# Performance work log

Hardware: AMD Instinct MI355X
Metric: run time of the kernel (lower is better)

Reference implementation:

```python
import jax, jax.numpy as jnp
import numpy as np
import math

N_USER = 50000
N_ITEM = 50000
E_PER = 400000
F_IN = 128
F_OUT = 128
H = 4
D = F_OUT // H  # 32
NUM_ET = 2  # edge types: 0 = user->item, 1 = item->user


def setup_inputs() -> dict:
    key = jax.random.key(0)
    ks = jax.random.split(key, 16)
    s = 0.05  # weight scale to keep activations tame
    return {
        "x_user": jax.random.normal(ks[0], (N_USER, F_IN), jnp.float32),
        "x_item": jax.random.normal(ks[1], (N_ITEM, F_IN), jnp.float32),
        "W_kqv_user": jax.random.normal(ks[2], (F_IN, 3 * F_OUT), jnp.float32) * s,
        "b_kqv_user": jax.random.normal(ks[3], (3 * F_OUT,), jnp.float32) * s,
        "W_kqv_item": jax.random.normal(ks[4], (F_IN, 3 * F_OUT), jnp.float32) * s,
        "b_kqv_item": jax.random.normal(ks[5], (3 * F_OUT,), jnp.float32) * s,
        "Wk_rel": jax.random.normal(ks[6], (H * NUM_ET, D, D), jnp.float32) * s,
        "Wv_rel": jax.random.normal(ks[7], (H * NUM_ET, D, D), jnp.float32) * s,
        "W_out_user": jax.random.normal(ks[8], (F_OUT, F_OUT), jnp.float32) * s,
        "b_out_user": jax.random.normal(ks[9], (F_OUT,), jnp.float32) * s,
        "W_out_item": jax.random.normal(ks[10], (F_OUT, F_OUT), jnp.float32) * s,
        "b_out_item": jax.random.normal(ks[11], (F_OUT,), jnp.float32) * s,
        "skip_user": jnp.ones((1,), jnp.float32),
        "skip_item": jnp.ones((1,), jnp.float32),
        "p_rel_ui": jnp.ones((H,), jnp.float32),
        "p_rel_iu": jnp.ones((H,), jnp.float32),
        "edge_ui": jax.random.randint(ks[12], (2, E_PER), 0, N_USER, dtype=jnp.int32),
        "edge_iu": jax.random.randint(ks[13], (2, E_PER), 0, N_ITEM, dtype=jnp.int32),
    }


def _kqv(x, W, b):
    o = x @ W + b  # [N, 3F]
    k, q, v = o[:, :F_OUT], o[:, F_OUT:2 * F_OUT], o[:, 2 * F_OUT:]
    return (k.reshape(-1, H, D), q.reshape(-1, H, D), v.reshape(-1, H, D))


def _rel(x, Wrel, et):
    # HeteroLinear with type index h*NUM_ET + et per head (is_sorted layout)
    W = Wrel[jnp.arange(H) * NUM_ET + et]  # [H, D, D]
    return jnp.einsum('nhd,hde->nhe', x, W)


def reference(x_user, x_item, W_kqv_user, b_kqv_user, W_kqv_item, b_kqv_item,
              Wk_rel, Wv_rel, W_out_user, b_out_user, W_out_item, b_out_item,
              skip_user, skip_item, p_rel_ui, p_rel_iu, edge_ui, edge_iu):
    ku, qu, vu = _kqv(x_user, W_kqv_user, b_kqv_user)
    ki, qi, vi = _kqv(x_item, W_kqv_item, b_kqv_item)

    # per-edge-type relation transform of K/V (grouped GEMM by head x edge-type)
    k0, v0 = _rel(ku, Wk_rel, 0), _rel(vu, Wv_rel, 0)  # src of user->item
    k1, v1 = _rel(ki, Wk_rel, 1), _rel(vi, Wv_rel, 1)  # src of item->user

    q_all = jnp.concatenate([qu, qi], 0)  # dst offsets: user=0, item=N_USER
    n_tot = N_USER + N_ITEM

    src0, dst0 = edge_ui[0], edge_ui[1] + N_USER
    src1, dst1 = edge_iu[0], edge_iu[1]

    kj = jnp.concatenate([k0[src0], k1[src1]], 0)  # [E, H, D]
    vj = jnp.concatenate([v0[src0], v1[src1]], 0)  # [E, H, D]
    dst = jnp.concatenate([dst0, dst1], 0)         # [E]
    p = jnp.concatenate([jnp.broadcast_to(p_rel_ui, (E_PER, H)),
                         jnp.broadcast_to(p_rel_iu, (E_PER, H))], 0)

    qe = q_all[dst]                                  # [E, H, D]
    alpha = (qe * kj).sum(-1) * p / math.sqrt(D)     # [E, H]

    # segment softmax over destination nodes (PyG softmax: max-shift, +1e-16)
    amax = jax.ops.segment_max(alpha, dst, num_segments=n_tot)
    a = jnp.exp(alpha - amax[dst])
    denom = jax.ops.segment_sum(a, dst, num_segments=n_tot)
    a = a / (denom[dst] + 1e-16)

    out = jax.ops.segment_sum(vj * a[:, :, None], dst, num_segments=n_tot)
    out = out.reshape(n_tot, F_OUT)
    out_u, out_i = out[:N_USER], out[N_USER:]

    g = lambda t: jax.nn.gelu(t, approximate=False)
    a_u = g(out_u) @ W_out_user + b_out_user
    a_i = g(out_i) @ W_out_item + b_out_item

    su = jax.nn.sigmoid(skip_user)  # out_channels == in_channels -> skip blend
    si = jax.nn.sigmoid(skip_item)
    return (su * a_u + (1.0 - su) * x_user,
            si * a_i + (1.0 - si) * x_item)
```

## Files before the change

### kernel.cpp

```cpp
#include <hip/hip_runtime.h>
#include <hip/hip_bf16.h>
#include <math.h>

#define N_USERS 50000
#define N_ITEMS 50000
#define NN      100000
#define E_PER_  400000
#define E_TOT   800000
#define FDIM    128
#define NH      4
#define HD      32
#define SCAN_CHUNK 1024
#define SCAN_NB    ((NN + SCAN_CHUNK - 1) / SCAN_CHUNK)
#define KQV_NB  ((N_USERS + 127) / 128)

typedef __attribute__((ext_vector_type(8))) short bfrag;
typedef __attribute__((ext_vector_type(4))) float f32x4;

__device__ __forceinline__ float gelu_exact(float x) {
    return 0.5f * x * (1.0f + erff(x * 0.70710678118654752f));
}
__device__ __forceinline__ unsigned short f2bf(float f) {
    unsigned u = __float_as_uint(f);
    unsigned r = u + 0x7fffu + ((u >> 16) & 1u);
    return (unsigned short)(r >> 16);
}
__device__ __forceinline__ void unpack8(uint4 u, float* f) {
    f[0] = __uint_as_float(u.x << 16); f[1] = __uint_as_float(u.x & 0xffff0000u);
    f[2] = __uint_as_float(u.y << 16); f[3] = __uint_as_float(u.y & 0xffff0000u);
    f[4] = __uint_as_float(u.z << 16); f[5] = __uint_as_float(u.z & 0xffff0000u);
    f[6] = __uint_as_float(u.w << 16); f[7] = __uint_as_float(u.w & 0xffff0000u);
}

__global__ void prep_kqv(
    const float* __restrict__ W_u, const float* __restrict__ b_u,
    const float* __restrict__ W_i, const float* __restrict__ b_i,
    const float* __restrict__ Wk_rel, const float* __restrict__ Wv_rel,
    unsigned short* __restrict__ Wt_u, float* __restrict__ bias_u,
    unsigned short* __restrict__ Wt_i, float* __restrict__ bias_i)
{
    const int et = blockIdx.x >> 9 ? 1 : (blockIdx.x >= 384);
    const int n = blockIdx.x - et * 384;
    const int k = threadIdx.x;
    const float* W = et ? W_i : W_u;
    const float* b = et ? b_i : b_u;
    unsigned short* Wt = et ? Wt_i : Wt_u;
    float* bias_f = et ? bias_i : bias_u;
    float s;
    if (n < 128) {
        int h = n >> 5, e = n & 31;
        const float* wr = Wk_rel + (size_t)(h * 2 + et) * 1024 + e;
        const float* wc = W + (size_t)k * 384 + h * 32;
        s = 0.f;
        for (int d = 0; d < 32; ++d) s = fmaf(wc[d], wr[d * 32], s);
        if (k == 0) {
            float bs = 0.f;
            for (int d = 0; d < 32; ++d) bs = fmaf(b[h * 32 + d], wr[d * 32], bs);
            bias_f[n] = bs;
        }
    } else if (n < 256) {
        s = W[(size_t)k * 384 + n];
        if (k == 0) bias_f[n] = b[n];
    } else {
        int h = (n - 256) >> 5, e = (n - 256) & 31;
        const float* wr = Wv_rel + (size_t)(h * 2 + et) * 1024 + e;
        const float* wc = W + (size_t)k * 384 + 256 + h * 32;
        s = 0.f;
        for (int d = 0; d < 32; ++d) s = fmaf(wc[d], wr[d * 32], s);
        if (k == 0) {
            float bs = 0.f;
            for (int d = 0; d < 32; ++d) bs = fmaf(b[256 + h * 32 + d], wr[d * 32], bs);
            bias_f[n] = bs;
        }
    }
    Wt[(size_t)n * 128 + k] = f2bf(s);
}

__global__ void prep_wo(
    const float* __restrict__ W_u, unsigned short* __restrict__ Wt_u,
    const float* __restrict__ W_i, unsigned short* __restrict__ Wt_i)
{
    int i = blockIdx.x * blockDim.x + threadIdx.x;
    int side = i >= 128 * 128;
    int j = i - side * 128 * 128;
    if (j >= 128 * 128) return;
    int nrow = j >> 7, k = j & 127;
    const float* W = side ? W_i : W_u;
    unsigned short* Wt = side ? Wt_i : Wt_u;
    Wt[j] = f2bf(W[(size_t)k * 128 + nrow]);
}

__global__ __launch_bounds__(256, 2) void kqv_mfma(
    const float* __restrict__ X_u, const unsigned short* __restrict__ Wt_u,
    const float* __restrict__ bias_u,
    const float* __restrict__ X_i, const unsigned short* __restrict__ Wt_i,
    const float* __restrict__ bias_i,
    unsigned short* __restrict__ kk_b,
    unsigned short* __restrict__ q_b,
    unsigned short* __restrict__ vv_b)
{
    __shared__ unsigned short Xs[128 * 128];
    __shared__ unsigned short Ws[128 * 128];
    const int t = threadIdx.x;
    const int side = blockIdx.x >= KQV_NB;
    const int m0 = (blockIdx.x - side * KQV_NB) * 128;
    const float* X = side ? X_i : X_u;
    const unsigned short* Wt = side ? Wt_i : Wt_u;
    const float* bias = side ? bias_i : bias_u;
    const int side_off = side ? N_USERS : 0;
    const int M = N_USERS;

    for (int c = t; c < 128 * 16; c += 256) {
        int r = c >> 4, sub = c & 15;
        int row = m0 + r;
        float4 a = make_float4(0.f, 0.f, 0.f, 0.f);
        float4 b4 = make_float4(0.f, 0.f, 0.f, 0.f);
        if (row < M) {
            a  = *reinterpret_cast<const float4*>(X + (size_t)row * 128 + sub * 8);
            b4 = *reinterpret_cast<const float4*>(X + (size_t)row * 128 + sub * 8 + 4);
        }
        uint4 pk;
        pk.x = (unsigned)f2bf(a.x)  | ((unsigned)f2bf(a.y)  << 16);
        pk.y = (unsigned)f2bf(a.z)  | ((unsigned)f2bf(a.w)  << 16);
        pk.z = (unsigned)f2bf(b4.x) | ((unsigned)f2bf(b4.y) << 16);
        pk.w = (unsigned)f2bf(b4.z) | ((unsigned)f2bf(b4.w) << 16);
        int dst = r * 256 + ((sub * 16) ^ ((r & 7) << 4));
        *reinterpret_cast<uint4*>(reinterpret_cast<char*>(Xs) + dst) = pk;
    }
    for (int c = t; c < 128 * 16; c += 256) {
        int r = c >> 4, sub = c & 15;
        uint4 v = *reinterpret_cast<const uint4*>(
            reinterpret_cast<const char*>(Wt) + (size_t)r * 256 + sub * 16);
        int dst = r * 256 + ((sub * 16) ^ ((r & 7) << 4));
        *reinterpret_cast<uint4*>(reinterpret_cast<char*>(Ws) + dst) = v;
    }
    __syncthreads();

    const int wave = t >> 6, lane = t & 63;
    const int lr = lane & 15, lg = lane >> 4;

    bfrag am[2][4];
    #pragma unroll
    for (int mt = 0; mt < 2; ++mt)
        #pragma unroll
        for (int ks = 0; ks < 4; ++ks) {
            int row = wave * 32 + mt * 16 + lr;
            int off = row * 256 + ((ks * 64 + lg * 16) ^ ((row & 7) << 4));
            am[mt][ks] = *reinterpret_cast<const bfrag*>(
                reinterpret_cast<const char*>(Xs) + off);
        }

    #pragma unroll
    for (int ch = 0; ch < 3; ++ch) {
        if (ch) {
            __syncthreads();
            for (int c = t; c < 128 * 16; c += 256) {
                int r = c >> 4, sub = c & 15;
                uint4 v = *reinterpret_cast<const uint4*>(
                    reinterpret_cast<const char*>(Wt) + (size_t)(ch * 128 + r) * 256 + sub * 16);
                int dst = r * 256 + ((sub * 16) ^ ((r & 7) << 4));
                *reinterpret_cast<uint4*>(reinterpret_cast<char*>(Ws) + dst) = v;
            }
            __syncthreads();
        }

        f32x4 acc[2][8];
        const f32x4 zero = {0.f, 0.f, 0.f, 0.f};
        #pragma unroll
        for (int mt = 0; mt < 2; ++mt)
            #pragma unroll
            for (int nt = 0; nt < 8; ++nt) acc[mt][nt] = zero;

        #pragma unroll
        for (int nt = 0; nt < 8; ++nt) {
            bfrag bt[4];
            int row = nt * 16 + lr;
            #pragma unroll
            for (int ks = 0; ks < 4; ++ks) {
                int off = row * 256 + ((ks * 64 + lg * 16) ^ ((row & 7) << 4));
                bt[ks] = *reinterpret_cast<const bfrag*>(
                    reinterpret_cast<const char*>(Ws) + off);
            }
            #pragma unroll
            for (int mt = 0; mt < 2; ++mt)
                #pragma unroll
                for (int ks = 0; ks < 4; ++ks)
                    acc[mt][nt] = __builtin_amdgcn_mfma_f32_16x16x32_bf16(
                        am[mt][ks], bt[ks], acc[mt][nt], 0, 0, 0);
        }

        unsigned short* arr = (ch == 0) ? kk_b : (ch == 1) ? q_b : vv_b;
        #pragma unroll
        for (int nt = 0; nt < 8; ++nt) {
            int ic = nt * 16 + lr;
            float bv = bias[ch * 128 + ic];
            #pragma unroll
            for (int mt = 0; mt < 2; ++mt)
                #pragma unroll
                for (int r = 0; r < 4; ++r) {
                    int row = m0 + wave * 32 + mt * 16 + lg * 4 + r;
                    if (row < M)
                        arr[(size_t)(side_off + row) * 128 + ic] = f2bf(acc[mt][nt][r] + bv);
                }
        }
    }
}

__device__ __forceinline__ void edge_src_dst(
    int e, const int* __restrict__ edge_ui, const int* __restrict__ edge_iu,
    int& src, int& dst)
{
    if (e < E_PER_) {
        src = edge_ui[e];
        dst = edge_ui[E_PER_ + e] + N_USERS;
    } else {
        int e2 = e - E_PER_;
        src = N_USERS + edge_iu[e2];
        dst = edge_iu[E_PER_ + e2];
    }
}

__global__ __launch_bounds__(256) void hist_kernel(
    const int* __restrict__ edge_ui, const int* __restrict__ edge_iu,
    int* __restrict__ cnt)
{
    int e = blockIdx.x * blockDim.x + threadIdx.x;
    if (e >= E_TOT) return;
    int src, dst;
    edge_src_dst(e, edge_ui, edge_iu, src, dst);
    atomicAdd(cnt + dst, 1);
}

__global__ __launch_bounds__(256) void scan1_kernel(
    const int* __restrict__ cnt, int* __restrict__ base, int* __restrict__ bsum)
{
    __shared__ int ssum[256];
    const int t = threadIdx.x;
    const int i0 = blockIdx.x * SCAN_CHUNK + t * 4;
    int v[4];
    #pragma unroll
    for (int j = 0; j < 4; ++j) v[j] = (i0 + j < NN) ? cnt[i0 + j] : 0;
    int tsum = v[0] + v[1] + v[2] + v[3];
    ssum[t] = tsum;
    __syncthreads();
    int run = tsum;
    for (int off = 1; off < 256; off <<= 1) {
        int o = (t >= off) ? ssum[t - off] : 0;
        __syncthreads();
        run += o;
        ssum[t] = run;
        __syncthreads();
    }
    int excl = run - tsum;
    int p = excl;
    #pragma unroll
    for (int j = 0; j < 4; ++j) {
        if (i0 + j < NN) base[i0 + j] = p;
        p += v[j];
    }
    if (t == 255) bsum[blockIdx.x] = run;
}

__global__ void scan2_kernel(int* __restrict__ bsum)
{
    const int lane = threadIdx.x;
    int a = (lane < SCAN_NB) ? bsum[lane] : 0;
    int b = (64 + lane < SCAN_NB) ? bsum[64 + lane] : 0;
    int sa = a, sb = b;
    for (int off = 1; off < 64; off <<= 1) {
        int ta = __shfl_up(sa, off);
        int tb = __shfl_up(sb, off);
        if (lane >= off) { sa += ta; sb += tb; }
    }
    int total0 = __shfl(sa, 63);
    if (lane < SCAN_NB) bsum[lane] = sa - a;
    if (64 + lane < SCAN_NB) bsum[64 + lane] = total0 + sb - b;
}

__global__ __launch_bounds__(256) void scan3_kernel(
    int* __restrict__ base, const int* __restrict__ bsum, int* __restrict__ cursor)
{
    int i = blockIdx.x * blockDim.x + threadIdx.x;
    if (i >= NN) return;
    int b = base[i] + bsum[i >> 10];
    base[i] = b;
    cursor[i] = b;
}

__global__ __launch_bounds__(256) void fill_kernel(
    const int* __restrict__ edge_ui, const int* __restrict__ edge_iu,
    int* __restrict__ cursor, int* __restrict__ esrc)
{
    int e = blockIdx.x * blockDim.x + threadIdx.x;
    if (e >= E_TOT) return;
    int src, dst;
    edge_src_dst(e, edge_ui, edge_iu, src, dst);
    int pos = atomicAdd(cursor + dst, 1);
    esrc[pos] = src;
}

__global__ __launch_bounds__(256) void attn_fused(
    const unsigned short* __restrict__ q_b, const unsigned short* __restrict__ kk_b,
    const unsigned short* __restrict__ vv_b,
    const int* __restrict__ base, const int* __restrict__ cnt,
    const int* __restrict__ esrc,
    const float* __restrict__ p_ui, const float* __restrict__ p_iu,
    unsigned short* __restrict__ oa)
{
    const int wid  = (blockIdx.x * blockDim.x + threadIdx.x) >> 6;
    const int lane = threadIdx.x & 63;
    const int nw   = (gridDim.x * blockDim.x) >> 6;
    const int g    = lane >> 4;
    const int p    = lane & 15;
    const int h    = p >> 2;
    const float rsd = 0.17677669529663687f;
    const float pu = p_ui[h], pi = p_iu[h];

    for (int n = wid; n < NN; n += nw) {
        const float pr = (n >= N_USERS) ? pu : pi;
        float qf[8];
        unpack8(*reinterpret_cast<const uint4*>(q_b + (size_t)n * 128 + p * 8), qf);
        float m = -INFINITY, l = 0.f;
        float acc[8] = {0.f, 0.f, 0.f, 0.f, 0.f, 0.f, 0.f, 0.f};
        const int s0 = base[n], c = cnt[n];

        if (c > 0) {
            bool valid = g < c;
            int src = esrc[s0 + (valid ? g : 0)];
            uint4 k4 = *reinterpret_cast<const uint4*>(kk_b + (size_t)src * 128 + p * 8);
            uint4 v4 = *reinterpret_cast<const uint4*>(vv_b + (size_t)src * 128 + p * 8);

            for (int j = 0; j < c; j += 4) {
                uint4 k4n, v4n;
                bool validn = false;
                if (j + 4 < c) {
                    int jn = j + 4 + g;
                    validn = jn < c;
                    int srcn = esrc[s0 + (validn ? jn : 0)];
                    k4n = *reinterpret_cast<const uint4*>(kk_b + (size_t)srcn * 128 + p * 8);
                    v4n = *reinterpret_cast<const uint4*>(vv_b + (size_t)srcn * 128 + p * 8);
                }

                float kf[8];
                unpack8(k4, kf);
                float s = qf[0] * kf[0];
                #pragma unroll
                for (int i = 1; i < 8; ++i) s = fmaf(qf[i], kf[i], s);
                s += __shfl_xor(s, 1);
                s += __shfl_xor(s, 2);
                float al = valid ? s * pr * rsd : -INFINITY;
                float amx = fmaxf(al, __shfl_xor(al, 16));
                amx = fmaxf(amx, __shfl_xor(amx, 32));
                if (__any(amx > m + 8.f)) {
                    float nm = fmaxf(m, amx);
                    float scale = __expf(m - nm);
                    l *= scale;
                    #pragma unroll
                    for (int i = 0; i < 8; ++i) acc[i] *= scale;
                    m = nm;
                }
                float w = __expf(al - m);
                l += w;
                float vf[8];
                unpack8(v4, vf);
                #pragma unroll
                for (int i = 0; i < 8; ++i) acc[i] = fmaf(w, vf[i], acc[i]);

                k4 = k4n; v4 = v4n; valid = validn;
            }
        }

        l += __shfl_xor(l, 16); l += __shfl_xor(l, 32);
        #pragma unroll
        for (int i = 0; i < 8; ++i) {
            acc[i] += __shfl_xor(acc[i], 16);
            acc[i] += __shfl_xor(acc[i], 32);
        }
        if (g == 0) {
            float inv = 1.0f / (l + 1e-16f);
            uint4 pk;
            unsigned o[4];
            #pragma unroll
            for (int i = 0; i < 4; ++i) {
                float lo = gelu_exact(acc[2 * i] * inv);
                float hi = gelu_exact(acc[2 * i + 1] * inv);
                o[i] = (unsigned)f2bf(lo) | ((unsigned)f2bf(hi) << 16);
            }
            pk.x = o[0]; pk.y = o[1]; pk.z = o[2]; pk.w = o[3];
            *reinterpret_cast<uint4*>(oa + (size_t)n * 128 + p * 8) = pk;
        }
    }
}

__global__ __launch_bounds__(256, 2) void final_mfma(
    const unsigned short* __restrict__ oa,
    const float* __restrict__ x_u, const unsigned short* __restrict__ Wt_u,
    const float* __restrict__ bo_u, const float* __restrict__ skip_u,
    const float* __restrict__ x_i, const unsigned short* __restrict__ Wt_i,
    const float* __restrict__ bo_i, const float* __restrict__ skip_i,
    float* __restrict__ out)
{
    __shared__ unsigned short Ws[128 * 128];
    __shared__ unsigned short Gs[128 * 128];
    const int t = threadIdx.x;
    const int side = blockIdx.x >= KQV_NB;
    const int m0 = (blockIdx.x - side * KQV_NB) * 128;
    const float* x = side ? x_i : x_u;
    const unsigned short* Wt = side ? Wt_i : Wt_u;
    const float* bo = side ? bo_i : bo_u;
    const float* skip = side ? skip_i : skip_u;
    const int row_off = side ? N_USERS : 0;
    const int M = N_USERS;

    for (int c = t; c < 128 * 16; c += 256) {
        int r = c >> 4, sub = c & 15;
        uint4 v = *reinterpret_cast<const uint4*>(
            reinterpret_cast<const char*>(Wt) + r * 256 + sub * 16);
        int dst = r * 256 + ((sub * 16) ^ ((r & 7) << 4));
        *reinterpret_cast<uint4*>(reinterpret_cast<char*>(Ws) + dst) = v;
    }
    for (int c = t; c < 128 * 16; c += 256) {
        int r = c >> 4, sub = c & 15;
        int row = m0 + r;
        uint4 v = make_uint4(0u, 0u, 0u, 0u);
        if (row < M)
            v = *reinterpret_cast<const uint4*>(
                reinterpret_cast<const char*>(oa) + (size_t)(row_off + row) * 256 + sub * 16);
        int dst = r * 256 + ((sub * 16) ^ ((r & 7) << 4));
        *reinterpret_cast<uint4*>(reinterpret_cast<char*>(Gs) + dst) = v;
    }
    __syncthreads();

    const int wave = t >> 6, lane = t & 63;
    const int lr = lane & 15, lg = lane >> 4;

    bfrag am[2][4];
    #pragma unroll
    for (int mt = 0; mt < 2; ++mt)
        #pragma unroll
        for (int ks = 0; ks < 4; ++ks) {
            int row = wave * 32 + mt * 16 + lr;
            int off = row * 256 + ((ks * 64 + lg * 16) ^ ((row & 7) << 4));
            am[mt][ks] = *reinterpret_cast<const bfrag*>(
                reinterpret_cast<const char*>(Gs) + off);
        }

    f32x4 acc[2][8];
    const f32x4 zero = {0.f, 0.f, 0.f, 0.f};
    #pragma unroll
    for (int mt = 0; mt < 2; ++mt)
        #pragma unroll
        for (int nt = 0; nt < 8; ++nt) acc[mt][nt] = zero;

    #pragma unroll
    for (int nt = 0; nt < 8; ++nt) {
        bfrag bt[4];
        int row = nt * 16 + lr;
        #pragma unroll
        for (int ks = 0; ks < 4; ++ks) {
            int off = row * 256 + ((ks * 64 + lg * 16) ^ ((row & 7) << 4));
            bt[ks] = *reinterpret_cast<const bfrag*>(
                reinterpret_cast<const char*>(Ws) + off);
        }
        #pragma unroll
        for (int mt = 0; mt < 2; ++mt)
            #pragma unroll
            for (int ks = 0; ks < 4; ++ks)
                acc[mt][nt] = __builtin_amdgcn_mfma_f32_16x16x32_bf16(
                    am[mt][ks], bt[ks], acc[mt][nt], 0, 0, 0);
    }

    const float sg = 1.0f / (1.0f + expf(-skip[0]));
    #pragma unroll
    for (int nt = 0; nt < 8; ++nt) {
        int col = nt * 16 + lr;
        float bv = bo[col];
        #pragma unroll
        for (int mt = 0; mt < 2; ++mt)
            #pragma unroll
            for (int r = 0; r < 4; ++r) {
                int row = m0 + wave * 32 + mt * 16 + lg * 4 + r;
                if (row < M) {
                    float xv = x[(size_t)row * 128 + col];
                    out[(size_t)(row_off + row) * 128 + col] =
                        sg * (acc[mt][nt][r] + bv) + (1.f - sg) * xv;
                }
            }
    }
}

extern "C" void kernel_launch(void* const* d_in, const int* in_sizes, int n_in,
                              void* d_out, int out_size, void* d_ws, size_t ws_size,
                              hipStream_t stream)
{
    const float* x_user     = (const float*)d_in[0];
    const float* x_item     = (const float*)d_in[1];
    const float* W_kqv_user = (const float*)d_in[2];
    const float* b_kqv_user = (const float*)d_in[3];
    const float* W_kqv_item = (const float*)d_in[4];
    const float* b_kqv_item = (const float*)d_in[5];
    const float* Wk_rel     = (const float*)d_in[6];
    const float* Wv_rel     = (const float*)d_in[7];
    const float* W_out_user = (const float*)d_in[8];
    const float* b_out_user = (const float*)d_in[9];
    const float* W_out_item = (const float*)d_in[10];
    const float* b_out_item = (const float*)d_in[11];
    const float* skip_user  = (const float*)d_in[12];
    const float* skip_item  = (const float*)d_in[13];
    const float* p_ui       = (const float*)d_in[14];
    const float* p_iu       = (const float*)d_in[15];
    const int*   edge_ui    = (const int*)d_in[16];
    const int*   edge_iu    = (const int*)d_in[17];

    const size_t NODE_F = (size_t)NN * FDIM;
    char* w = (char*)d_ws;
    size_t off = 0;
    auto alloc = [&](size_t bytes) {
        char* p = w + off;
        off += (bytes + 255) & ~(size_t)255;
        return p;
    };
    unsigned short* q_b   = (unsigned short*)alloc(NODE_F * 2);
    unsigned short* kk_b  = (unsigned short*)alloc(NODE_F * 2);
    unsigned short* vv_b  = (unsigned short*)alloc(NODE_F * 2);
    unsigned short* oa_b  = (unsigned short*)alloc(NODE_F * 2);
    int* esrc   = (int*)alloc((size_t)E_TOT * 4);
    int* cnt    = (int*)alloc((size_t)NN * 4);
    int* base   = (int*)alloc((size_t)NN * 4);
    int* cursor = (int*)alloc((size_t)NN * 4);
    int* bsum   = (int*)alloc((size_t)SCAN_NB * 4);
    unsigned short* Wt_u   = (unsigned short*)alloc(384 * 128 * 2);
    unsigned short* Wt_i   = (unsigned short*)alloc(384 * 128 * 2);
    float*          bias_u = (float*)alloc(384 * 4);
    float*          bias_i = (float*)alloc(384 * 4);
    unsigned short* Wo_u   = (unsigned short*)alloc(128 * 128 * 2);
    unsigned short* Wo_i   = (unsigned short*)alloc(128 * 128 * 2);

    prep_kqv<<<768, 128, 0, stream>>>(W_kqv_user, b_kqv_user, W_kqv_item, b_kqv_item,
                                      Wk_rel, Wv_rel, Wt_u, bias_u, Wt_i, bias_i);
    prep_wo<<<128, 256, 0, stream>>>(W_out_user, Wo_u, W_out_item, Wo_i);

    kqv_mfma<<<2 * KQV_NB, 256, 0, stream>>>(x_user, Wt_u, bias_u,
                                             x_item, Wt_i, bias_i,
                                             kk_b, q_b, vv_b);

    hipMemsetAsync(cnt, 0, (size_t)NN * 4, stream);
    hist_kernel<<<(E_TOT + 255) / 256, 256, 0, stream>>>(edge_ui, edge_iu, cnt);
    scan1_kernel<<<SCAN_NB, 256, 0, stream>>>(cnt, base, bsum);
    scan2_kernel<<<1, 64, 0, stream>>>(bsum);
    scan3_kernel<<<(NN + 255) / 256, 256, 0, stream>>>(base, bsum, cursor);
    fill_kernel<<<(E_TOT + 255) / 256, 256, 0, stream>>>(edge_ui, edge_iu, cursor, esrc);

    attn_fused<<<2048, 256, 0, stream>>>(q_b, kk_b, vv_b, base, cnt, esrc,
                                         p_ui, p_iu, oa_b);

    final_mfma<<<2 * KQV_NB, 256, 0, stream>>>(
        oa_b, x_user, Wo_u, b_out_user, skip_user,
        x_item, Wo_i, b_out_item, skip_item, (float*)d_out);
}
```

Measured before the change: 282.0 us.

## Pre-swizzle weights into MFMA fragment order and drop LDS staging in GEMMs

Weights are pre-packed into per-lane MFMA fragment order, so the kqv and final GEMM kernels load A and B fragments straight from global memory into registers instead of staging through shared memory with barriers. The MFMA operands are swapped so each lane's accumulator holds 4 consecutive columns, which allows vectorized bias loads and packed uint2/float4 output stores. Launch bounds rise to 3 blocks per CU since no LDS is used. The cost is that every wave re-reads the weight fragments from cache, and there is more register pressure from the double-buffered B fragments.

```diff
diff --git a/kernel.cpp b/kernel.cpp
--- a/kernel.cpp
+++ b/kernel.cpp
@@ -31,20 +31,25 @@
     f[4] = __uint_as_float(u.z << 16); f[5] = __uint_as_float(u.z & 0xffff0000u);
     f[6] = __uint_as_float(u.w << 16); f[7] = __uint_as_float(u.w & 0xffff0000u);
 }
+__device__ __forceinline__ size_t wfrag_idx(int n, int k) {
+    int ch = n >> 7, nt = (n >> 4) & 7, lr = n & 15;
+    int ks = k >> 5, lg = (k >> 3) & 3, e = k & 7;
+    return ((size_t)(((ch * 8 + nt) * 4 + ks) * 64 + lg * 16 + lr)) * 8 + e;
+}
 
 __global__ void prep_kqv(
     const float* __restrict__ W_u, const float* __restrict__ b_u,
     const float* __restrict__ W_i, const float* __restrict__ b_i,
     const float* __restrict__ Wk_rel, const float* __restrict__ Wv_rel,
-    unsigned short* __restrict__ Wt_u, float* __restrict__ bias_u,
-    unsigned short* __restrict__ Wt_i, float* __restrict__ bias_i)
-{
-    const int et = blockIdx.x >> 9 ? 1 : (blockIdx.x >= 384);
+    unsigned short* __restrict__ F_u, float* __restrict__ bias_u,
+    unsigned short* __restrict__ F_i, float* __restrict__ bias_i)
+{
+    const int et = blockIdx.x >= 384;
     const int n = blockIdx.x - et * 384;
     const int k = threadIdx.x;
     const float* W = et ? W_i : W_u;
     const float* b = et ? b_i : b_u;
-    unsigned short* Wt = et ? Wt_i : Wt_u;
+    unsigned short* F = et ? F_i : F_u;
     float* bias_f = et ? bias_i : bias_u;
     float s;
     if (n < 128) {
@@ -73,97 +78,68 @@
             bias_f[n] = bs;
         }
     }
-    Wt[(size_t)n * 128 + k] = f2bf(s);
+    F[wfrag_idx(n, k)] = f2bf(s);
 }
 
 __global__ void prep_wo(
-    const float* __restrict__ W_u, unsigned short* __restrict__ Wt_u,
-    const float* __restrict__ W_i, unsigned short* __restrict__ Wt_i)
+    const float* __restrict__ W_u, unsigned short* __restrict__ F_u,
+    const float* __restrict__ W_i, unsigned short* __restrict__ F_i)
 {
     int i = blockIdx.x * blockDim.x + threadIdx.x;
     int side = i >= 128 * 128;
     int j = i - side * 128 * 128;
     if (j >= 128 * 128) return;
-    int nrow = j >> 7, k = j & 127;
+    int n = j >> 7, k = j & 127;
     const float* W = side ? W_i : W_u;
-    unsigned short* Wt = side ? Wt_i : Wt_u;
-    Wt[j] = f2bf(W[(size_t)k * 128 + nrow]);
-}
-
-__global__ __launch_bounds__(256, 2) void kqv_mfma(
-    const float* __restrict__ X_u, const unsigned short* __restrict__ Wt_u,
+    unsigned short* F = side ? F_i : F_u;
+    F[wfrag_idx(n, k)] = f2bf(W[(size_t)k * 128 + n]);
+}
+
+__global__ __launch_bounds__(256, 3) void kqv_mfma(
+    const float* __restrict__ X_u, const unsigned short* __restrict__ F_u,
     const float* __restrict__ bias_u,
-    const float* __restrict__ X_i, const unsigned short* __restrict__ Wt_i,
+    const float* __restrict__ X_i, const unsigned short* __restrict__ F_i,
     const float* __restrict__ bias_i,
     unsigned short* __restrict__ kk_b,
     unsigned short* __restrict__ q_b,
     unsigned short* __restrict__ vv_b)
 {
-    __shared__ unsigned short Xs[128 * 128];
-    __shared__ unsigned short Ws[128 * 128];
     const int t = threadIdx.x;
     const int side = blockIdx.x >= KQV_NB;
     const int m0 = (blockIdx.x - side * KQV_NB) * 128;
     const float* X = side ? X_i : X_u;
-    const unsigned short* Wt = side ? Wt_i : Wt_u;
+    const unsigned short* F = side ? F_i : F_u;
     const float* bias = side ? bias_i : bias_u;
     const int side_off = side ? N_USERS : 0;
     const int M = N_USERS;
 
-    for (int c = t; c < 128 * 16; c += 256) {
-        int r = c >> 4, sub = c & 15;
-        int row = m0 + r;
-        float4 a = make_float4(0.f, 0.f, 0.f, 0.f);
-        float4 b4 = make_float4(0.f, 0.f, 0.f, 0.f);
-        if (row < M) {
-            a  = *reinterpret_cast<const float4*>(X + (size_t)row * 128 + sub * 8);
-            b4 = *reinterpret_cast<const float4*>(X + (size_t)row * 128 + sub * 8 + 4);
-        }
-        uint4 pk;
-        pk.x = (unsigned)f2bf(a.x)  | ((unsigned)f2bf(a.y)  << 16);
-        pk.y = (unsigned)f2bf(a.z)  | ((unsigned)f2bf(a.w)  << 16);
-        pk.z = (unsigned)f2bf(b4.x) | ((unsigned)f2bf(b4.y) << 16);
-        pk.w = (unsigned)f2bf(b4.z) | ((unsigned)f2bf(b4.w) << 16);
-        int dst = r * 256 + ((sub * 16) ^ ((r & 7) << 4));
-        *reinterpret_cast<uint4*>(reinterpret_cast<char*>(Xs) + dst) = pk;
-    }
-    for (int c = t; c < 128 * 16; c += 256) {
-        int r = c >> 4, sub = c & 15;
-        uint4 v = *reinterpret_cast<const uint4*>(
-            reinterpret_cast<const char*>(Wt) + (size_t)r * 256 + sub * 16);
-        int dst = r * 256 + ((sub * 16) ^ ((r & 7) << 4));
-        *reinterpret_cast<uint4*>(reinterpret_cast<char*>(Ws) + dst) = v;
-    }
-    __syncthreads();
-
     const int wave = t >> 6, lane = t & 63;
     const int lr = lane & 15, lg = lane >> 4;
+    const int rbase = m0 + wave * 32;
 
     bfrag am[2][4];
     #pragma unroll
     for (int mt = 0; mt < 2; ++mt)
         #pragma unroll
         for (int ks = 0; ks < 4; ++ks) {
-            int row = wave * 32 + mt * 16 + lr;
-            int off = row * 256 + ((ks * 64 + lg * 16) ^ ((row & 7) << 4));
-            am[mt][ks] = *reinterpret_cast<const bfrag*>(
-                reinterpret_cast<const char*>(Xs) + off);
+            int row = rbase + mt * 16 + lr;
+            float4 a = make_float4(0.f, 0.f, 0.f, 0.f);
+            float4 b4 = make_float4(0.f, 0.f, 0.f, 0.f);
+            if (row < M) {
+                const float* px = X + (size_t)row * 128 + ks * 32 + lg * 8;
+                a  = *reinterpret_cast<const float4*>(px);
+                b4 = *reinterpret_cast<const float4*>(px + 4);
+            }
+            uint4 pk;
+            pk.x = (unsigned)f2bf(a.x)  | ((unsigned)f2bf(a.y)  << 16);
+            pk.y = (unsigned)f2bf(a.z)  | ((unsigned)f2bf(a.w)  << 16);
+            pk.z = (unsigned)f2bf(b4.x) | ((unsigned)f2bf(b4.y) << 16);
+            pk.w = (unsigned)f2bf(b4.z) | ((unsigned)f2bf(b4.w) << 16);
+            am[mt][ks] = *reinterpret_cast<bfrag*>(&pk);
         }
 
     #pragma unroll
     for (int ch = 0; ch < 3; ++ch) {
-        if (ch) {
-            __syncthreads();
-            for (int c = t; c < 128 * 16; c += 256) {
-                int r = c >> 4, sub = c & 15;
-                uint4 v = *reinterpret_cast<const uint4*>(
-                    reinterpret_cast<const char*>(Wt) + (size_t)(ch * 128 + r) * 256 + sub * 16);
-                int dst = r * 256 + ((sub * 16) ^ ((r & 7) << 4));
-                *reinterpret_cast<uint4*>(reinterpret_cast<char*>(Ws) + dst) = v;
-            }
-            __syncthreads();
-        }
-
         f32x4 acc[2][8];
         const f32x4 zero = {0.f, 0.f, 0.f, 0.f};
         #pragma unroll
@@ -171,37 +147,47 @@
             #pragma unroll
             for (int nt = 0; nt < 8; ++nt) acc[mt][nt] = zero;
 
+        bfrag bc[4], bn[4];
+        #pragma unroll
+        for (int ks = 0; ks < 4; ++ks)
+            bc[ks] = *reinterpret_cast<const bfrag*>(
+                F + ((size_t)((ch * 8 + 0) * 4 + ks) * 64 + lane) * 8);
+
         #pragma unroll
         for (int nt = 0; nt < 8; ++nt) {
-            bfrag bt[4];
-            int row = nt * 16 + lr;
-            #pragma unroll
-            for (int ks = 0; ks < 4; ++ks) {
-                int off = row * 256 + ((ks * 64 + lg * 16) ^ ((row & 7) << 4));
-                bt[ks] = *reinterpret_cast<const bfrag*>(
-                    reinterpret_cast<const char*>(Ws) + off);
+            if (nt < 7) {
+                #pragma unroll
+                for (int ks = 0; ks < 4; ++ks)
+                    bn[ks] = *reinterpret_cast<const bfrag*>(
+                        F + ((size_t)((ch * 8 + nt + 1) * 4 + ks) * 64 + lane) * 8);
             }
             #pragma unroll
             for (int mt = 0; mt < 2; ++mt)
                 #pragma unroll
                 for (int ks = 0; ks < 4; ++ks)
                     acc[mt][nt] = __builtin_amdgcn_mfma_f32_16x16x32_bf16(
-                        am[mt][ks], bt[ks], acc[mt][nt], 0, 0, 0);
+                        bc[ks], am[mt][ks], acc[mt][nt], 0, 0, 0);
+            #pragma unroll
+            for (int ks = 0; ks < 4; ++ks) bc[ks] = bn[ks];
         }
 
         unsigned short* arr = (ch == 0) ? kk_b : (ch == 1) ? q_b : vv_b;
         #pragma unroll
         for (int nt = 0; nt < 8; ++nt) {
-            int ic = nt * 16 + lr;
-            float bv = bias[ch * 128 + ic];
-            #pragma unroll
-            for (int mt = 0; mt < 2; ++mt)
-                #pragma unroll
-                for (int r = 0; r < 4; ++r) {
-                    int row = m0 + wave * 32 + mt * 16 + lg * 4 + r;
-                    if (row < M)
-                        arr[(size_t)(side_off + row) * 128 + ic] = f2bf(acc[mt][nt][r] + bv);
+            float4 bv = *reinterpret_cast<const float4*>(bias + ch * 128 + nt * 16 + lg * 4);
+            #pragma unroll
+            for (int mt = 0; mt < 2; ++mt) {
+                int row = rbase + mt * 16 + lr;
+                if (row < M) {
+                    unsigned lo = (unsigned)f2bf(acc[mt][nt][0] + bv.x)
+                                | ((unsigned)f2bf(acc[mt][nt][1] + bv.y) << 16);
+                    unsigned hi = (unsigned)f2bf(acc[mt][nt][2] + bv.z)
+                                | ((unsigned)f2bf(acc[mt][nt][3] + bv.w) << 16);
+                    uint2 st = make_uint2(lo, hi);
+                    *reinterpret_cast<uint2*>(
+                        arr + (size_t)(side_off + row) * 128 + nt * 16 + lg * 4) = st;
                 }
+            }
         }
     }
 }
@@ -392,57 +378,39 @@
     }
 }
 
-__global__ __launch_bounds__(256, 2) void final_mfma(
+__global__ __launch_bounds__(256, 3) void final_mfma(
     const unsigned short* __restrict__ oa,
-    const float* __restrict__ x_u, const unsigned short* __restrict__ Wt_u,
+    const float* __restrict__ x_u, const unsigned short* __restrict__ F_u,
     const float* __restrict__ bo_u, const float* __restrict__ skip_u,
-    const float* __restrict__ x_i, const unsigned short* __restrict__ Wt_i,
+    const float* __restrict__ x_i, const unsigned short* __restrict__ F_i,
     const float* __restrict__ bo_i, const float* __restrict__ skip_i,
     float* __restrict__ out)
 {
-    __shared__ unsigned short Ws[128 * 128];
-    __shared__ unsigned short Gs[128 * 128];
     const int t = threadIdx.x;
     const int side = blockIdx.x >= KQV_NB;
     const int m0 = (blockIdx.x - side * KQV_NB) * 128;
     const float* x = side ? x_i : x_u;
-    const unsigned short* Wt = side ? Wt_i : Wt_u;
+    const unsigned short* F = side ? F_i : F_u;
     const float* bo = side ? bo_i : bo_u;
     const float* skip = side ? skip_i : skip_u;
     const int row_off = side ? N_USERS : 0;
     const int M = N_USERS;
 
-    for (int c = t; c < 128 * 16; c += 256) {
-        int r = c >> 4, sub = c & 15;
-        uint4 v = *reinterpret_cast<const uint4*>(
-            reinterpret_cast<const char*>(Wt) + r * 256 + sub * 16);
-        int dst = r * 256 + ((sub * 16) ^ ((r & 7) << 4));
-        *reinterpret_cast<uint4*>(reinterpret_cast<char*>(Ws) + dst) = v;
-    }
-    for (int c = t; c < 128 * 16; c += 256) {
-        int r = c >> 4, sub = c & 15;
-        int row = m0 + r;
-        uint4 v = make_uint4(0u, 0u, 0u, 0u);
-        if (row < M)
-            v = *reinterpret_cast<const uint4*>(
-                reinterpret_cast<const char*>(oa) + (size_t)(row_off + row) * 256 + sub * 16);
-        int dst = r * 256 + ((sub * 16) ^ ((r & 7) << 4));
-        *reinterpret_cast<uint4*>(reinterpret_cast<char*>(Gs) + dst) = v;
-    }
-    __syncthreads();
-
     const int wave = t >> 6, lane = t & 63;
     const int lr = lane & 15, lg = lane >> 4;
+    const int rbase = m0 + wave * 32;
 
     bfrag am[2][4];
+    const bfrag bz = {0, 0, 0, 0, 0, 0, 0, 0};
     #pragma unroll
     for (int mt = 0; mt < 2; ++mt)
         #pragma unroll
         for (int ks = 0; ks < 4; ++ks) {
-            int row = wave * 32 + mt * 16 + lr;
-            int off = row * 256 + ((ks * 64 + lg * 16) ^ ((row & 7) << 4));
-            am[mt][ks] = *reinterpret_cast<const bfrag*>(
-                reinterpret_cast<const char*>(Gs) + off);
+            int row = rbase + mt * 16 + lr;
+            am[mt][ks] = (row < M)
+                ? *reinterpret_cast<const bfrag*>(
+                      oa + (size_t)(row_off + row) * 128 + ks * 32 + lg * 8)
+                : bz;
         }
 
     f32x4 acc[2][8];
@@ -452,40 +420,49 @@
         #pragma unroll
         for (int nt = 0; nt < 8; ++nt) acc[mt][nt] = zero;
 
+    bfrag bc[4], bn[4];
+    #pragma unroll
+    for (int ks = 0; ks < 4; ++ks)
+        bc[ks] = *reinterpret_cast<const bfrag*>(
+            F + ((size_t)(0 * 4 + ks) * 64 + lane) * 8);
+
     #pragma unroll
     for (int nt = 0; nt < 8; ++nt) {
-        bfrag bt[4];
-        int row = nt * 16 + lr;
-        #pragma unroll
-        for (int ks = 0; ks < 4; ++ks) {
-            int off = row * 256 + ((ks * 64 + lg * 16) ^ ((row & 7) << 4));
-            bt[ks] = *reinterpret_cast<const bfrag*>(
-                reinterpret_cast<const char*>(Ws) + off);
+        if (nt < 7) {
+            #pragma unroll
+            for (int ks = 0; ks < 4; ++ks)
+                bn[ks] = *reinterpret_cast<const bfrag*>(
+                    F + ((size_t)((nt + 1) * 4 + ks) * 64 + lane) * 8);
         }
         #pragma unroll
         for (int mt = 0; mt < 2; ++mt)
             #pragma unroll
             for (int ks = 0; ks < 4; ++ks)
                 acc[mt][nt] = __builtin_amdgcn_mfma_f32_16x16x32_bf16(
-                    am[mt][ks], bt[ks], acc[mt][nt], 0, 0, 0);
+                    bc[ks], am[mt][ks], acc[mt][nt], 0, 0, 0);
+        #pragma unroll
+        for (int ks = 0; ks < 4; ++ks) bc[ks] = bn[ks];
     }
 
     const float sg = 1.0f / (1.0f + expf(-skip[0]));
     #pragma unroll
     for (int nt = 0; nt < 8; ++nt) {
-        int col = nt * 16 + lr;
-        float bv = bo[col];
-        #pragma unroll
-        for (int mt = 0; mt < 2; ++mt)
-            #pragma unroll
-            for (int r = 0; r < 4; ++r) {
-                int row = m0 + wave * 32 + mt * 16 + lg * 4 + r;
-                if (row < M) {
-                    float xv = x[(size_t)row * 128 + col];
-                    out[(size_t)(row_off + row) * 128 + col] =
-                        sg * (acc[mt][nt][r] + bv) + (1.f - sg) * xv;
-                }
+        float4 bv = *reinterpret_cast<const float4*>(bo + nt * 16 + lg * 4);
+        #pragma unroll
+        for (int mt = 0; mt < 2; ++mt) {
+            int row = rbase + mt * 16 + lr;
+            if (row < M) {
+                float4 xv = *reinterpret_cast<const float4*>(
+                    x + (size_t)row * 128 + nt * 16 + lg * 4);
+                float4 res;
+                res.x = sg * (acc[mt][nt][0] + bv.x) + (1.f - sg) * xv.x;
+                res.y = sg * (acc[mt][nt][1] + bv.y) + (1.f - sg) * xv.y;
+                res.z = sg * (acc[mt][nt][2] + bv.z) + (1.f - sg) * xv.z;
+                res.w = sg * (acc[mt][nt][3] + bv.w) + (1.f - sg) * xv.w;
+                *reinterpret_cast<float4*>(
+                    out + (size_t)(row_off + row) * 128 + nt * 16 + lg * 4) = res;
             }
+        }
     }
 }
 
@@ -529,19 +506,19 @@
     int* base   = (int*)alloc((size_t)NN * 4);
     int* cursor = (int*)alloc((size_t)NN * 4);
     int* bsum   = (int*)alloc((size_t)SCAN_NB * 4);
-    unsigned short* Wt_u   = (unsigned short*)alloc(384 * 128 * 2);
-    unsigned short* Wt_i   = (unsigned short*)alloc(384 * 128 * 2);
+    unsigned short* F_u    = (unsigned short*)alloc(384 * 128 * 2);
+    unsigned short* F_i    = (unsigned short*)alloc(384 * 128 * 2);
     float*          bias_u = (float*)alloc(384 * 4);
     float*          bias_i = (float*)alloc(384 * 4);
-    unsigned short* Wo_u   = (unsigned short*)alloc(128 * 128 * 2);
-    unsigned short* Wo_i   = (unsigned short*)alloc(128 * 128 * 2);
+    unsigned short* Fo_u   = (unsigned short*)alloc(128 * 128 * 2);
+    unsigned short* Fo_i   = (unsigned short*)alloc(128 * 128 * 2);
 
     prep_kqv<<<768, 128, 0, stream>>>(W_kqv_user, b_kqv_user, W_kqv_item, b_kqv_item,
-                                      Wk_rel, Wv_rel, Wt_u, bias_u, Wt_i, bias_i);
-    prep_wo<<<128, 256, 0, stream>>>(W_out_user, Wo_u, W_out_item, Wo_i);
-
-    kqv_mfma<<<2 * KQV_NB, 256, 0, stream>>>(x_user, Wt_u, bias_u,
-                                             x_item, Wt_i, bias_i,
+                                      Wk_rel, Wv_rel, F_u, bias_u, F_i, bias_i);
+    prep_wo<<<128, 256, 0, stream>>>(W_out_user, Fo_u, W_out_item, Fo_i);
+
+    kqv_mfma<<<2 * KQV_NB, 256, 0, stream>>>(x_user, F_u, bias_u,
+                                             x_item, F_i, bias_i,
                                              kk_b, q_b, vv_b);
 
     hipMemsetAsync(cnt, 0, (size_t)NN * 4, stream);
@@ -555,6 +532,6 @@
                                          p_ui, p_iu, oa_b);
 
     final_mfma<<<2 * KQV_NB, 256, 0, stream>>>(
-        oa_b, x_user, Wo_u, b_out_user, skip_user,
-        x_item, Wo_i, b_out_item, skip_item, (float*)d_out);
-}
+        oa_b, x_user, Fo_u, b_out_user, skip_user,
+        x_item, Fo_i, b_out_item, skip_item, (float*)d_out);
+}
```

Result: faster. 242.0 us (-14.2%).
